# Optimization experiments

Hardware: AMD Instinct MI355X
Metric: run time of the kernel (lower is better)

The kernel has to match this reference:

```python
import jax, jax.numpy as jnp
import numpy as np

N = 12288
IN_F = 256
OUT_F = 128
ALPHA = 0.2  # LeakyReLU negative slope


def setup_inputs() -> dict:
    key = jax.random.key(0)
    k_x, k_adj, k_w, k_a1, k_a2 = jax.random.split(key, 5)
    x = jax.random.normal(k_x, (N, IN_F), dtype=jnp.float32)
    adj = jax.random.randint(k_adj, (N, N), 0, 2, dtype=jnp.int32)
    # Learned params (nn.Linear without bias). Kaiming-uniform-ish init scale.
    W = jax.random.normal(k_w, (IN_F, OUT_F), dtype=jnp.float32) / np.sqrt(IN_F)
    a1 = jax.random.normal(k_a1, (OUT_F,), dtype=jnp.float32) / np.sqrt(OUT_F)
    a2 = jax.random.normal(k_a2, (OUT_F,), dtype=jnp.float32) / np.sqrt(OUT_F)
    return {"x": x, "adj": adj, "W": W, "a1": a1, "a2": a2}


def reference(x, adj, W, a1, a2):
    # h = tran(x): [N, OUT_F]
    h = x @ W
    # e[i, j] = att1(h)[j] + att2(h)[i]  (unsqueeze(0) + unsqueeze(1))
    s1 = h @ a1  # [N]
    s2 = h @ a2  # [N]
    e = s1[None, :] + s2[:, None]            # [N, N]
    e = jnp.where(e > 0, e, ALPHA * e)       # LeakyReLU
    e = jnp.where(adj > 0, e, -jnp.inf)      # mask non-edges
    attn = jax.nn.softmax(e, axis=1)         # row softmax (dropout=0 / eval)
    return attn @ h                          # [N, OUT_F]
```

## Files before the change

### kernel.cpp

```cpp
#include <hip/hip_runtime.h>
#include <hip/hip_bf16.h>
#include <hip/hip_fp16.h>

constexpr int NR = 12288;
constexpr int KF = 256;
constexpr int DF = 128;
constexpr int CH = 16;
constexpr int CW = NR / CH;
constexpr int NSTEP = CW / 32;
constexpr int ROWS = 128;
constexpr int BMW = NR / 32;
#define NEGBIG (-1e30f)

typedef __attribute__((ext_vector_type(8))) __bf16 bf16x8;
typedef __attribute__((ext_vector_type(4))) float  f32x4;

__device__ __forceinline__ unsigned short f2bf(float f) {
    union { float f; unsigned u; } v; v.f = f;
    unsigned r = v.u + 0x7FFFu + ((v.u >> 16) & 1u);
    return (unsigned short)(r >> 16);
}

__device__ __forceinline__ void gload16(const void* g, void* l) {
    __builtin_amdgcn_global_load_lds(
        (const __attribute__((address_space(1))) void*)g,
        (__attribute__((address_space(3))) void*)l, 16, 0, 0);
}

__global__ __launch_bounds__(256) void k_compress(
    const int* __restrict__ adj, unsigned* __restrict__ bm)
{
    const int lane = threadIdx.x & 63;
    const unsigned sh = (lane & 7) * 4;
    size_t i = (size_t)blockIdx.x * 256 + threadIdx.x;
    const size_t total4 = (size_t)NR * NR / 4;
    const size_t stride = (size_t)gridDim.x * 256;
    const int4* a4 = (const int4*)adj;
    for (; i < total4; i += stride) {
        int4 a = a4[i];
        unsigned nib = (unsigned)(a.x > 0) | ((unsigned)(a.y > 0) << 1)
                     | ((unsigned)(a.z > 0) << 2) | ((unsigned)(a.w > 0) << 3);
        unsigned v = nib << sh;
        v |= __shfl_xor(v, 1);
        v |= __shfl_xor(v, 2);
        v |= __shfl_xor(v, 4);
        if ((lane & 7) == 0) bm[i >> 3] = v;
    }
}

__global__ __launch_bounds__(256) void k_gemm_h(
    const float* __restrict__ x, const float* __restrict__ W,
    const float* __restrict__ a1, const float* __restrict__ a2,
    unsigned short* __restrict__ hbT, float* __restrict__ s1, float* __restrict__ s2)
{
    __shared__ __align__(16) float xs[64][65];
    __shared__ __align__(16) float ws[64][132];
    const int t  = threadIdx.x;
    const int tx = t & 15, ty = t >> 4;
    const int rowbase = blockIdx.x * 64;

    float acc[4][8];
#pragma unroll
    for (int i = 0; i < 4; ++i)
#pragma unroll
        for (int j = 0; j < 8; ++j) acc[i][j] = 0.f;

    for (int kt = 0; kt < KF; kt += 64) {
        {
            int row = t >> 2, k0 = (t & 3) * 16;
            const float4* src = (const float4*)(x + (size_t)(rowbase + row) * KF + kt + k0);
            float4 v0 = src[0], v1 = src[1], v2 = src[2], v3 = src[3];
            xs[row][k0+ 0]=v0.x; xs[row][k0+ 1]=v0.y; xs[row][k0+ 2]=v0.z; xs[row][k0+ 3]=v0.w;
            xs[row][k0+ 4]=v1.x; xs[row][k0+ 5]=v1.y; xs[row][k0+ 6]=v1.z; xs[row][k0+ 7]=v1.w;
            xs[row][k0+ 8]=v2.x; xs[row][k0+ 9]=v2.y; xs[row][k0+10]=v2.z; xs[row][k0+11]=v2.w;
            xs[row][k0+12]=v3.x; xs[row][k0+13]=v3.y; xs[row][k0+14]=v3.z; xs[row][k0+15]=v3.w;
        }
        {
            int k = t >> 2, c0 = (t & 3) * 32;
            const float4* src = (const float4*)(W + (size_t)(kt + k) * DF + c0);
#pragma unroll
            for (int j = 0; j < 8; ++j)
                *(float4*)&ws[k][c0 + j * 4] = src[j];
        }
        __syncthreads();
#pragma unroll 4
        for (int k = 0; k < 64; ++k) {
            float xv[4];
#pragma unroll
            for (int ri = 0; ri < 4; ++ri) xv[ri] = xs[ty * 4 + ri][k];
            float4 w0 = *(float4*)&ws[k][tx * 8];
            float4 w1 = *(float4*)&ws[k][tx * 8 + 4];
#pragma unroll
            for (int ri = 0; ri < 4; ++ri) {
                acc[ri][0] += xv[ri] * w0.x; acc[ri][1] += xv[ri] * w0.y;
                acc[ri][2] += xv[ri] * w0.z; acc[ri][3] += xv[ri] * w0.w;
                acc[ri][4] += xv[ri] * w1.x; acc[ri][5] += xv[ri] * w1.y;
                acc[ri][6] += xv[ri] * w1.z; acc[ri][7] += xv[ri] * w1.w;
            }
        }
        __syncthreads();
    }
#pragma unroll
    for (int ci = 0; ci < 8; ++ci) {
        int col = tx * 8 + ci;
        ushort4 u;
        u.x = f2bf(acc[0][ci]); u.y = f2bf(acc[1][ci]);
        u.z = f2bf(acc[2][ci]); u.w = f2bf(acc[3][ci]);
        *(ushort4*)(hbT + (size_t)col * NR + rowbase + ty * 4) = u;
    }
    float4 a1lo = *(const float4*)(a1 + tx * 8), a1hi = *(const float4*)(a1 + tx * 8 + 4);
    float4 a2lo = *(const float4*)(a2 + tx * 8), a2hi = *(const float4*)(a2 + tx * 8 + 4);
#pragma unroll
    for (int ri = 0; ri < 4; ++ri) {
        float p1 = acc[ri][0]*a1lo.x + acc[ri][1]*a1lo.y + acc[ri][2]*a1lo.z + acc[ri][3]*a1lo.w
                 + acc[ri][4]*a1hi.x + acc[ri][5]*a1hi.y + acc[ri][6]*a1hi.z + acc[ri][7]*a1hi.w;
        float p2 = acc[ri][0]*a2lo.x + acc[ri][1]*a2lo.y + acc[ri][2]*a2lo.z + acc[ri][3]*a2lo.w
                 + acc[ri][4]*a2hi.x + acc[ri][5]*a2hi.y + acc[ri][6]*a2hi.z + acc[ri][7]*a2hi.w;
#pragma unroll
        for (int off = 8; off > 0; off >>= 1) {
            p1 += __shfl_xor(p1, off);
            p2 += __shfl_xor(p2, off);
        }
        if (tx == 0) {
            s1[rowbase + ty * 4 + ri] = p1;
            s2[rowbase + ty * 4 + ri] = p2;
        }
    }
}

__global__ __launch_bounds__(1024) void k_gmax(
    const float* __restrict__ s1, float* __restrict__ gmax)
{
    __shared__ float red[16];
    const int t = threadIdx.x;
    float m = NEGBIG;
    const float4* s4 = (const float4*)s1;
    for (int i = t; i < NR / 4; i += 1024) {
        float4 v = s4[i];
        m = fmaxf(fmaxf(v.x, v.y), fmaxf(fmaxf(v.z, v.w), m));
    }
#pragma unroll
    for (int off = 32; off > 0; off >>= 1) m = fmaxf(m, __shfl_xor(m, off));
    if ((t & 63) == 0) red[t >> 6] = m;
    __syncthreads();
    if (t < 16) {
        m = red[t];
#pragma unroll
        for (int off = 8; off > 0; off >>= 1) m = fmaxf(m, __shfl_xor(m, off));
        if (t == 0) gmax[0] = m;
    }
}

__global__ __launch_bounds__(512, 4) void k_flash(
    const unsigned* __restrict__ bm, const unsigned short* __restrict__ hbT,
    const float* __restrict__ s1, const float* __restrict__ s2,
    const float* __restrict__ gmaxp,
    __half* __restrict__ num, float* __restrict__ lC)
{
    __shared__ __align__(16) unsigned short hbtring[3][4096];
    __shared__ __align__(16) unsigned       bmlds[ROWS][28];
    __shared__ __align__(16) float          s1lds[CW];

    const int t    = threadIdx.x;
    const int wid  = t >> 6, lane = t & 63;
    const int r    = lane & 15, g = lane >> 4;
    const int rowb = blockIdx.x * ROWS;
    const int prow = rowb + wid * 16 + r;
    const int chunk = blockIdx.y;
    const int j0 = chunk * CW;

    if (t < CW / 4) *(float4*)&s1lds[t * 4] = *(const float4*)(s1 + j0 + t * 4);
#pragma unroll
    for (int i = 0; i < 2; ++i) {
        int idx = i * 512 + t;
        if (idx < 768) {
            int brow = idx / 6, bk = idx % 6;
            uint4 w = *(const uint4*)(bm + (size_t)(rowb + brow) * BMW + chunk * NSTEP + bk * 4);
            *(uint4*)&bmlds[brow][bk * 4] = w;
        }
    }

    const float gm  = gmaxp[0];
    const float s2r = s2[prow];
    const float zub = s2r + gm;
    const float Mi  = fmaxf(zub, 0.2f * zub);

    const int hrow  = wid * 16 + (lane >> 2);
    const int hcol8 = ((lane & 3) ^ ((lane >> 3) & 3)) * 8;
    const unsigned short* hgp0 = hbT + (size_t)hrow * NR + j0 + hcol8;
    const int hldso0 = wid * 16 * 64;
    const int h_base = r * 64 + ((g ^ ((r >> 1) & 3)) * 16);

#define ISSUE(st) do { \
        const int sl_ = (st) % 3; \
        const size_t go_ = (size_t)(((st) % NSTEP) * 32); \
        gload16(hgp0 + go_, (char*)&hbtring[sl_][0] + hldso0); \
    } while (0)

    float lsum = 0.f;
    f32x4 acc[8];
#pragma unroll
    for (int f = 0; f < 8; ++f) acc[f] = f32x4{0.f, 0.f, 0.f, 0.f};

    ISSUE(0);
    ISSUE(1);

    const unsigned* bmrow = &bmlds[wid * 16 + r][0];
    const unsigned gsh = g * 8;

    for (int j = 0; j < NSTEP; ++j) {
        asm volatile("s_waitcnt vmcnt(1) lgkmcnt(0)" ::: "memory");
        __builtin_amdgcn_s_barrier();
        __builtin_amdgcn_sched_barrier(0);
        ISSUE(j + 2);

        const unsigned mw = bmrow[j] >> gsh;
        const float4 Sa = *(const float4*)&s1lds[j * 32 + g * 8];
        const float4 Sb = *(const float4*)&s1lds[j * 32 + g * 8 + 4];

        bf16x8 pf;
#define PROC(bi, ss, idx) { \
            float t0 = (ss) + s2r; \
            float lr = fmaxf(t0, 0.2f * t0); \
            float q  = __expf(lr - Mi); \
            float p  = ((mw >> (bi)) & 1u) ? q : 0.f; \
            lsum += p; \
            pf[idx] = (__bf16)p; }
        PROC(0, Sa.x, 0) PROC(1, Sa.y, 1)
        PROC(2, Sa.z, 2) PROC(3, Sa.w, 3)
        PROC(4, Sb.x, 4) PROC(5, Sb.y, 5)
        PROC(6, Sb.z, 6) PROC(7, Sb.w, 7)
#undef PROC

        const int sl = j % 3;
        const char* hb = (const char*)&hbtring[sl][0] + h_base;
#pragma unroll
        for (int f = 0; f < 8; ++f) {
            bf16x8 bfr = *(const bf16x8*)(hb + f * 1024);
            acc[f] = __builtin_amdgcn_mfma_f32_16x16x32_bf16(pf, bfr, acc[f], 0, 0, 0);
        }
    }
#undef ISSUE

    lsum += __shfl_xor(lsum, 16);
    lsum += __shfl_xor(lsum, 32);
    if (g == 0) lC[(size_t)chunk * NR + prow] = lsum;

    __half* nb = num + (size_t)chunk * NR * DF;
#pragma unroll
    for (int f = 0; f < 8; ++f)
#pragma unroll
        for (int q = 0; q < 4; ++q) {
            int row = rowb + wid * 16 + g * 4 + q;
            nb[(size_t)row * DF + f * 16 + r] = __float2half(acc[f][q]);
        }
}

__global__ __launch_bounds__(256) void k_comb(
    const __half* __restrict__ num, const float* __restrict__ lC,
    float* __restrict__ out)
{
    const int t   = threadIdx.x;
    const int row = blockIdx.x * 2 + (t >> 7);
    const int f   = t & 127;
    float L = 0.f, o = 0.f;
    for (int c = 0; c < CH; ++c) {
        L += lC[(size_t)c * NR + row];
        o += __half2float(num[(size_t)c * NR * DF + (size_t)row * DF + f]);
    }
    out[(size_t)row * DF + f] = o / L;
}

extern "C" void kernel_launch(void* const* d_in, const int* in_sizes, int n_in,
                              void* d_out, int out_size, void* d_ws, size_t ws_size,
                              hipStream_t stream)
{
    const float* x   = (const float*)d_in[0];
    const int*   adj = (const int*)d_in[1];
    const float* W   = (const float*)d_in[2];
    const float* a1  = (const float*)d_in[3];
    const float* a2  = (const float*)d_in[4];
    float* out = (float*)d_out;

    char* p = (char*)d_ws;
    unsigned short* hbT = (unsigned short*)p; p += (size_t)DF * NR * 2;
    unsigned*       bmw = (unsigned*)p;       p += (size_t)NR * BMW * 4;
    float*          s1  = (float*)p;          p += (size_t)NR * 4;
    float*          s2  = (float*)p;          p += (size_t)NR * 4;
    float*          gmx = (float*)p;          p += 256;
    __half*         numb = (__half*)p;        p += (size_t)CH * NR * DF * 2;
    float*          lC   = (float*)p;

    k_compress<<<2048, 256, 0, stream>>>(adj, bmw);
    k_gemm_h<<<NR / 64, 256, 0, stream>>>(x, W, a1, a2, hbT, s1, s2);
    k_gmax<<<1, 1024, 0, stream>>>(s1, gmx);
    k_flash<<<dim3(NR / ROWS, CH), 512, 0, stream>>>(bmw, hbT, s1, s2, gmx, numb, lC);
    k_comb<<<NR / 2, 256, 0, stream>>>(numb, lC, out);
}
```

Before: 222.7 us.

## Fuse global max into GEMM via atomicMax and double flash block rows

Removes the single-block k_gmax kernel by computing the s1 maximum inside k_gemm_h with an order-preserving unsigned atomicMax, initialised in k_compress. The flash kernel now processes 256 rows per block with 1024 threads, so each staged hbT tile is reused by twice as many rows. Only the first 8 waves issue the hbT loads, and the other waves wait on LDS only. The larger blocks may reduce occupancy and increase register pressure under the 1024-thread launch bound.

Measured after the change: 249.3 us. 12.0% more time.

```diff
diff --git a/kernel.cpp b/kernel.cpp
--- a/kernel.cpp
+++ b/kernel.cpp
@@ -8,7 +8,7 @@
 constexpr int CH = 16;
 constexpr int CW = NR / CH;
 constexpr int NSTEP = CW / 32;
-constexpr int ROWS = 128;
+constexpr int ROWS = 256;
 constexpr int BMW = NR / 32;
 #define NEGBIG (-1e30f)
 
@@ -27,9 +27,19 @@
         (__attribute__((address_space(3))) void*)l, 16, 0, 0);
 }
 
+__device__ __forceinline__ unsigned fmap(float f) {
+    unsigned b = __float_as_uint(f);
+    return (b & 0x80000000u) ? ~b : (b | 0x80000000u);
+}
+__device__ __forceinline__ float funmap(unsigned m) {
+    unsigned b = (m & 0x80000000u) ? (m ^ 0x80000000u) : ~m;
+    return __uint_as_float(b);
+}
+
 __global__ __launch_bounds__(256) void k_compress(
-    const int* __restrict__ adj, unsigned* __restrict__ bm)
-{
+    const int* __restrict__ adj, unsigned* __restrict__ bm, unsigned* __restrict__ gmxu)
+{
+    if (blockIdx.x == 0 && threadIdx.x == 0) gmxu[0] = 0u;
     const int lane = threadIdx.x & 63;
     const unsigned sh = (lane & 7) * 4;
     size_t i = (size_t)blockIdx.x * 256 + threadIdx.x;
@@ -51,12 +61,14 @@
 __global__ __launch_bounds__(256) void k_gemm_h(
     const float* __restrict__ x, const float* __restrict__ W,
     const float* __restrict__ a1, const float* __restrict__ a2,
-    unsigned short* __restrict__ hbT, float* __restrict__ s1, float* __restrict__ s2)
+    unsigned short* __restrict__ hbT, float* __restrict__ s1, float* __restrict__ s2,
+    unsigned* __restrict__ gmxu)
 {
     __shared__ __align__(16) float xs[64][65];
     __shared__ __align__(16) float ws[64][132];
     const int t  = threadIdx.x;
     const int tx = t & 15, ty = t >> 4;
+    const int lane = t & 63;
     const int rowbase = blockIdx.x * 64;
 
     float acc[4][8];
@@ -110,6 +122,7 @@
     }
     float4 a1lo = *(const float4*)(a1 + tx * 8), a1hi = *(const float4*)(a1 + tx * 8 + 4);
     float4 a2lo = *(const float4*)(a2 + tx * 8), a2hi = *(const float4*)(a2 + tx * 8 + 4);
+    float lmax = NEGBIG;
 #pragma unroll
     for (int ri = 0; ri < 4; ++ri) {
         float p1 = acc[ri][0]*a1lo.x + acc[ri][1]*a1lo.y + acc[ri][2]*a1lo.z + acc[ri][3]*a1lo.w
@@ -125,36 +138,17 @@
             s1[rowbase + ty * 4 + ri] = p1;
             s2[rowbase + ty * 4 + ri] = p2;
         }
-    }
-}
-
-__global__ __launch_bounds__(1024) void k_gmax(
-    const float* __restrict__ s1, float* __restrict__ gmax)
-{
-    __shared__ float red[16];
-    const int t = threadIdx.x;
-    float m = NEGBIG;
-    const float4* s4 = (const float4*)s1;
-    for (int i = t; i < NR / 4; i += 1024) {
-        float4 v = s4[i];
-        m = fmaxf(fmaxf(v.x, v.y), fmaxf(fmaxf(v.z, v.w), m));
-    }
-#pragma unroll
-    for (int off = 32; off > 0; off >>= 1) m = fmaxf(m, __shfl_xor(m, off));
-    if ((t & 63) == 0) red[t >> 6] = m;
-    __syncthreads();
-    if (t < 16) {
-        m = red[t];
-#pragma unroll
-        for (int off = 8; off > 0; off >>= 1) m = fmaxf(m, __shfl_xor(m, off));
-        if (t == 0) gmax[0] = m;
-    }
-}
-
-__global__ __launch_bounds__(512, 4) void k_flash(
+        lmax = fmaxf(lmax, p1);
+    }
+    lmax = fmaxf(lmax, __shfl_xor(lmax, 16));
+    lmax = fmaxf(lmax, __shfl_xor(lmax, 32));
+    if (lane == 0) atomicMax(gmxu, fmap(lmax));
+}
+
+__global__ __launch_bounds__(1024, 4) void k_flash(
     const unsigned* __restrict__ bm, const unsigned short* __restrict__ hbT,
     const float* __restrict__ s1, const float* __restrict__ s2,
-    const float* __restrict__ gmaxp,
+    const unsigned* __restrict__ gmxu,
     __half* __restrict__ num, float* __restrict__ lC)
 {
     __shared__ __align__(16) unsigned short hbtring[3][4096];
@@ -172,15 +166,15 @@
     if (t < CW / 4) *(float4*)&s1lds[t * 4] = *(const float4*)(s1 + j0 + t * 4);
 #pragma unroll
     for (int i = 0; i < 2; ++i) {
-        int idx = i * 512 + t;
-        if (idx < 768) {
+        int idx = i * 1024 + t;
+        if (idx < 1536) {
             int brow = idx / 6, bk = idx % 6;
             uint4 w = *(const uint4*)(bm + (size_t)(rowb + brow) * BMW + chunk * NSTEP + bk * 4);
             *(uint4*)&bmlds[brow][bk * 4] = w;
         }
     }
 
-    const float gm  = gmaxp[0];
+    const float gm  = funmap(gmxu[0]);
     const float s2r = s2[prow];
     const float zub = s2r + gm;
     const float Mi  = fmaxf(zub, 0.2f * zub);
@@ -194,7 +188,7 @@
 #define ISSUE(st) do { \
         const int sl_ = (st) % 3; \
         const size_t go_ = (size_t)(((st) % NSTEP) * 32); \
-        gload16(hgp0 + go_, (char*)&hbtring[sl_][0] + hldso0); \
+        if (wid < 8) gload16(hgp0 + go_, (char*)&hbtring[sl_][0] + hldso0); \
     } while (0)
 
     float lsum = 0.f;
@@ -209,7 +203,8 @@
     const unsigned gsh = g * 8;
 
     for (int j = 0; j < NSTEP; ++j) {
-        asm volatile("s_waitcnt vmcnt(1) lgkmcnt(0)" ::: "memory");
+        if (wid < 8) asm volatile("s_waitcnt vmcnt(1) lgkmcnt(0)" ::: "memory");
+        else         asm volatile("s_waitcnt lgkmcnt(0)" ::: "memory");
         __builtin_amdgcn_s_barrier();
         __builtin_amdgcn_sched_barrier(0);
         ISSUE(j + 2);
@@ -287,13 +282,12 @@
     unsigned*       bmw = (unsigned*)p;       p += (size_t)NR * BMW * 4;
     float*          s1  = (float*)p;          p += (size_t)NR * 4;
     float*          s2  = (float*)p;          p += (size_t)NR * 4;
-    float*          gmx = (float*)p;          p += 256;
+    unsigned*       gmxu = (unsigned*)p;      p += 256;
     __half*         numb = (__half*)p;        p += (size_t)CH * NR * DF * 2;
     float*          lC   = (float*)p;
 
-    k_compress<<<2048, 256, 0, stream>>>(adj, bmw);
-    k_gemm_h<<<NR / 64, 256, 0, stream>>>(x, W, a1, a2, hbT, s1, s2);
-    k_gmax<<<1, 1024, 0, stream>>>(s1, gmx);
-    k_flash<<<dim3(NR / ROWS, CH), 512, 0, stream>>>(bmw, hbT, s1, s2, gmx, numb, lC);
+    k_compress<<<2048, 256, 0, stream>>>(adj, bmw, gmxu);
+    k_gemm_h<<<NR / 64, 256, 0, stream>>>(x, W, a1, a2, hbT, s1, s2, gmxu);
+    k_flash<<<dim3(NR / ROWS, CH), 1024, 0, stream>>>(bmw, hbT, s1, s2, gmxu, numb, lC);
     k_comb<<<NR / 2, 256, 0, stream>>>(numb, lC, out);
 }
```
